# Kernel optimization log

Hardware: AMD Instinct MI355X
Metric: run time of the kernel (lower is better)

Reference implementation:

```python
import jax, jax.numpy as jnp
import numpy as np

N = 100000      # nodes
E = 1200000     # edges per relation
R = 3           # relations
D_IN = 64       # input_dim
HEAD = 4
HD = 16         # output_dim per head
HHD = HEAD * HD # head * output_dim
NEG_SLOPE = 0.01  # torch LeakyReLU default


def setup_inputs() -> dict:
    key = jax.random.key(0)
    ks = jax.random.split(key, 12)
    sc = 0.05
    h = jax.random.normal(ks[0], (N, D_IN), dtype=jnp.float32)
    src = jax.random.randint(ks[1], (R, E), 0, N, dtype=jnp.int32)
    dst = jax.random.randint(ks[2], (R, E), 0, N, dtype=jnp.int32)
    # shared RelationAware d_liner
    d_w = jax.random.normal(ks[3], (D_IN, HHD), dtype=jnp.float32) * sc
    d_b = jnp.zeros((HHD,), jnp.float32)
    # per-relation H_layer w_liner
    w_w = jax.random.normal(ks[4], (R, D_IN, HHD), dtype=jnp.float32) * sc
    w_b = jnp.zeros((R, HHD), jnp.float32)
    # per-relation attention Linear(3*hd, 1)
    atten_w = jax.random.normal(ks[5], (R, 3 * HD), dtype=jnp.float32) * sc
    atten_b = jnp.zeros((R,), jnp.float32)
    # per-relation Gate beta: (2*head*hd, 1)
    beta = jax.random.normal(ks[6], (R, 2 * HHD), dtype=jnp.float32) * sc
    # final combine liner: (R*head*hd -> head*hd)
    lin_w = jax.random.normal(ks[7], (R * HHD, HHD), dtype=jnp.float32) * sc
    lin_b = jnp.zeros((HHD,), jnp.float32)
    return dict(h=h, src=src, dst=dst, d_w=d_w, d_b=d_b, w_w=w_w, w_b=w_b,
                atten_w=atten_w, atten_b=atten_b, beta=beta, lin_w=lin_w, lin_b=lin_b)


def _relation(h, d_feat, s, t, w_w_r, w_b_r, atten_w_r, atten_b_r, beta_r):
    # H_layer forward for one relation; s/t are edge src/dst indices [E]
    hp = h @ w_w_r + w_b_r                       # [N, HHD] (w_liner)
    # RelationAware: tanh(src + dst + (src - dst)) == tanh(2*src)
    es = jnp.tanh(2.0 * d_feat[s])               # [E, HHD] per-edge edge_sum
    src_h = hp[s].reshape(E, HEAD, HD)
    dst_h = hp[t].reshape(E, HEAD, HD)
    es_h = es.reshape(E, HEAD, HD)
    # atten Linear(3*hd,1) on concat[src,dst,edge_s]: split weight, avoid concat
    wa = atten_w_r.reshape(3, HD)
    logits = src_h @ wa[0] + dst_h @ wa[1] + es_h @ wa[2] + atten_b_r  # [E, HEAD]
    alpha = jnp.where(logits >= 0, logits, NEG_SLOPE * logits)          # leaky_relu
    # segment softmax over incoming edges per destination, per head
    amax = jnp.full((N, HEAD), jnp.finfo(jnp.float32).min, jnp.float32).at[t].max(alpha)
    ex = jnp.exp(alpha - amax[t])                                        # [E, HEAD]
    denom = jax.ops.segment_sum(ex, t, num_segments=N)                   # [N, HEAD]
    w = ex / jnp.maximum(denom[t], 1e-20)
    out = jax.ops.segment_sum(w[..., None] * src_h, t, num_segments=N)   # [N, HEAD, HD]
    out = out.reshape(N, HHD)
    # mean of edge_sum over incoming edges per destination
    cnt = jax.ops.segment_sum(jnp.ones((E,), jnp.float32), t, num_segments=N)
    es_node = jax.ops.segment_sum(es, t, num_segments=N) / jnp.maximum(cnt, 1.0)[:, None]
    # Gate
    gate = jax.nn.sigmoid(jnp.concatenate([es_node, out], axis=1) @ beta_r[:, None])  # [N,1]
    return gate * out + (1.0 - gate) * hp


def reference(h, src, dst, d_w, d_b, w_w, w_b, atten_w, atten_b, beta, lin_w, lin_b):
    d_feat = h @ d_w + d_b                        # shared RelationAware d_liner, [N, HHD]
    hs = [
        _relation(h, d_feat, src[r], dst[r], w_w[r], w_b[r], atten_w[r], atten_b[r], beta[r])
        for r in range(R)
    ]
    x = jnp.concatenate(hs, axis=1)               # [N, R*HHD]; dropout p=0 -> identity
    return x @ lin_w + lin_b                      # [N, HHD]
```

## Files before the change

### kernel.cpp

```cpp
#include <hip/hip_runtime.h>

#define N_NODES 100000
#define N_EDGES 1200000
#define R_REL 3
#define RN (R_REL * N_NODES)
#define RE (R_REL * N_EDGES)

#define B_BITS 9
#define W_BKT 512
#define NB_R 196
#define K_BKT (R_REL * NB_R)
#define TILE_A 8192
#define NBLK_A ((RE + TILE_A - 1) / TILE_A)
#define NODE_BLKS 1024

typedef _Float16 half4v __attribute__((ext_vector_type(4)));

__device__ __forceinline__ float bcast(float v, int l) {
  return __int_as_float(__builtin_amdgcn_readlane(__float_as_int(v), l));
}

__device__ __forceinline__ int rel_of(int e) {
  return (e >= 2 * N_EDGES) ? 2 : (e >= N_EDGES ? 1 : 0);
}

__global__ __launch_bounds__(256) void k_hist(const int* __restrict__ dst,
                                              int* __restrict__ tot) {
  __shared__ int sh[K_BKT];
  int tid = threadIdx.x;
  for (int i = tid; i < K_BKT; i += 256) sh[i] = 0;
  __syncthreads();
  int base = blockIdx.x * TILE_A;
  int end = min(base + TILE_A, RE);
  for (int e = base + tid; e < end; e += 256) {
    atomicAdd(&sh[rel_of(e) * NB_R + (dst[e] >> B_BITS)], 1);
  }
  __syncthreads();
  for (int i = tid; i < K_BKT; i += 256) {
    int c = sh[i];
    if (c) atomicAdd(&tot[i], c);
  }
}

__global__ void k_scanK(const int* __restrict__ tot, int* __restrict__ BB,
                        int* __restrict__ cursor) {
  __shared__ int sd[256];
  int t = threadIdx.x;
  int v[3];
  int tots = 0;
#pragma unroll
  for (int q = 0; q < 3; q++) {
    int k = t * 3 + q;
    v[q] = (k < K_BKT) ? tot[k] : 0;
    tots += v[q];
  }
  sd[t] = tots;
  __syncthreads();
  for (int off = 1; off < 256; off <<= 1) {
    int x = (t >= off) ? sd[t - off] : 0;
    __syncthreads();
    sd[t] += x;
    __syncthreads();
  }
  int run = sd[t] - tots;
#pragma unroll
  for (int q = 0; q < 3; q++) {
    int k = t * 3 + q;
    if (k < K_BKT) {
      BB[k] = run;
      cursor[k] = run;
    }
    run += v[q];
  }
  if (t == 255) BB[K_BKT] = RE;
}

__global__ __launch_bounds__(256) void k_scatterA(const int* __restrict__ src,
                                                  const int* __restrict__ dst,
                                                  int* __restrict__ cursor,
                                                  unsigned int* __restrict__ rec) {
  __shared__ int sh[K_BKT];
  int tid = threadIdx.x;
  for (int i = tid; i < K_BKT; i += 256) sh[i] = 0;
  __syncthreads();
  int base = blockIdx.x * TILE_A;
  int end = min(base + TILE_A, RE);
  for (int e = base + tid; e < end; e += 256) {
    atomicAdd(&sh[rel_of(e) * NB_R + (dst[e] >> B_BITS)], 1);
  }
  __syncthreads();
  for (int i = tid; i < K_BKT; i += 256) {
    int c = sh[i];
    sh[i] = c ? atomicAdd(&cursor[i], c) : 0;
  }
  __syncthreads();
  for (int e = base + tid; e < end; e += 256) {
    int d = dst[e];
    int k = rel_of(e) * NB_R + (d >> B_BITS);
    int p = atomicAdd(&sh[k], 1);
    rec[p] = ((unsigned)src[e] << B_BITS) | (unsigned)(d & (W_BKT - 1));
  }
}

__global__ __launch_bounds__(256) void k_nb(
    const unsigned int* __restrict__ rec, const int* __restrict__ BB,
    int* __restrict__ P, int* __restrict__ ssrc,
    const float* __restrict__ h, const float* __restrict__ d_w,
    const float* __restrict__ d_b, const float* __restrict__ w_w,
    const float* __restrict__ w_b, const float* __restrict__ atten_w,
    const float* __restrict__ atten_b, const float* __restrict__ beta,
    _Float16* __restrict__ hp16, float* __restrict__ pk,
    float* __restrict__ adst) {
  __shared__ float sW[4 * 4096];
  __shared__ int cnt[W_BKT];
  __shared__ int sdx[256];
  int tid = threadIdx.x;
  if (blockIdx.x < K_BKT) {
    int kb = blockIdx.x;
    int r = kb / NB_R;
    int nb0 = (kb % NB_R) * W_BKT;
    int beg = BB[kb], end = BB[kb + 1];
    cnt[tid] = 0;
    cnt[256 + tid] = 0;
    __syncthreads();
    for (int e = beg + tid; e < end; e += 256)
      atomicAdd(&cnt[rec[e] & (W_BKT - 1)], 1);
    __syncthreads();
    int v0 = cnt[2 * tid], v1 = cnt[2 * tid + 1];
    int tot2 = v0 + v1;
    sdx[tid] = tot2;
    __syncthreads();
    for (int off = 1; off < 256; off <<= 1) {
      int x = (tid >= off) ? sdx[tid - off] : 0;
      __syncthreads();
      sdx[tid] += x;
      __syncthreads();
    }
    int run = sdx[tid] - tot2;
    int node0 = nb0 + 2 * tid;
    int pbase = r * N_NODES + node0;
    if (node0 < N_NODES) P[pbase] = beg + run;
    if (node0 + 1 < N_NODES) P[pbase + 1] = beg + run + v0;
    cnt[2 * tid] = beg + run;
    cnt[2 * tid + 1] = beg + run + v0;
    __syncthreads();
    for (int e = beg + tid; e < end; e += 256) {
      unsigned rc = rec[e];
      int p = atomicAdd(&cnt[rc & (W_BKT - 1)], 1);
      ssrc[p] = (int)(rc >> B_BITS);
    }
    return;
  }
  int nbid = blockIdx.x - K_BKT;
  for (int idx = tid; idx < 4096; idx += 256) {
    sW[idx] = d_w[idx];
    sW[4096 + idx] = w_w[idx];
    sW[8192 + idx] = w_w[4096 + idx];
    sW[12288 + idx] = w_w[8192 + idx];
  }
  __syncthreads();
  int lane = tid & 63, wid = tid >> 6;
  int wave = nbid * 4 + wid, nw = NODE_BLKS * 4;
  int k16 = lane & 15, hgrp = lane >> 4;
  float dbv = d_b[lane];
  float wbv0 = w_b[lane], wbv1 = w_b[64 + lane], wbv2 = w_b[128 + lane];
  float wa0[3], wa1[3], wa2[3], ab[3], bb[3];
#pragma unroll
  for (int r = 0; r < 3; r++) {
    wa0[r] = atten_w[r * 48 + k16];
    wa1[r] = atten_w[r * 48 + 16 + k16];
    wa2[r] = atten_w[r * 48 + 32 + k16];
    ab[r] = atten_b[r];
    bb[r] = beta[r * 128 + lane];
  }
  for (int g = wave; g < N_NODES / 8; g += nw) {
    int n0 = g * 8;
    float hr[8];
#pragma unroll
    for (int i = 0; i < 8; i++) hr[i] = h[(n0 + i) * 64 + lane];
    float acc[8][4];
#pragma unroll
    for (int i = 0; i < 8; i++) {
      acc[i][0] = dbv; acc[i][1] = wbv0; acc[i][2] = wbv1; acc[i][3] = wbv2;
    }
#pragma unroll 4
    for (int k = 0; k < 64; k++) {
      float w0 = sW[k * 64 + lane];
      float w1 = sW[4096 + k * 64 + lane];
      float w2 = sW[8192 + k * 64 + lane];
      float w3 = sW[12288 + k * 64 + lane];
#pragma unroll
      for (int i = 0; i < 8; i++) {
        float a = bcast(hr[i], k);
        acc[i][0] += a * w0; acc[i][1] += a * w1;
        acc[i][2] += a * w2; acc[i][3] += a * w3;
      }
    }
#pragma unroll
    for (int i = 0; i < 8; i++) {
      int n = n0 + i;
      float esv = tanhf(2.f * acc[i][0]);
#pragma unroll
      for (int r = 0; r < 3; r++) {
        int idxrn = r * N_NODES + n;
        float hpv = acc[i][1 + r];
        hp16[(size_t)idxrn * 64 + lane] = (_Float16)hpv;
        float cs = hpv * wa0[r] + esv * wa2[r];
        float cd = hpv * wa1[r];
#pragma unroll
        for (int m = 1; m < 16; m <<= 1) {
          cs += __shfl_xor(cs, m);
          cd += __shfl_xor(cd, m);
        }
        float sv = esv * bb[r];
#pragma unroll
        for (int m = 1; m < 64; m <<= 1) sv += __shfl_xor(sv, m);
        if (k16 == 0) {
          float2 rec2 = make_float2(cs + ab[r], sv);
          *reinterpret_cast<float2*>(&pk[(size_t)idxrn * 8 + hgrp * 2]) = rec2;
          adst[(size_t)idxrn * 4 + hgrp] = cd;
        }
      }
    }
  }
}

#define EDGE_BODY(EE, OA, DS, SD)                                          \
  {                                                                        \
    int s_ = ssrc[EE];                                                     \
    float2 pv_ = *reinterpret_cast<const float2*>(&pkr[s_ * 8 + head2]);   \
    half4v hv_ = *reinterpret_cast<const half4v*>(&hpr16[s_ * 64 + cq]);   \
    float a_ = pv_.x + adh;                                                \
    a_ = a_ >= 0.f ? a_ : 0.01f * a_;                                      \
    float ex_ = __expf(a_);                                                \
    OA.x += ex_ * (float)hv_.x;                                            \
    OA.y += ex_ * (float)hv_.y;                                            \
    OA.z += ex_ * (float)hv_.z;                                            \
    OA.w += ex_ * (float)hv_.w;                                            \
    DS += ex_;                                                             \
    SD += pv_.y;                                                           \
  }

__global__ __launch_bounds__(1024, 2) void k_fused(
    const _Float16* __restrict__ hp16, const float* __restrict__ pk,
    const float* __restrict__ adst, const int* __restrict__ P,
    const int* __restrict__ ssrc, const float* __restrict__ beta,
    const float* __restrict__ lin_w, const float* __restrict__ lin_b,
    float* __restrict__ out) {
  __shared__ __align__(16) float sLW[64 * 196];
  __shared__ __align__(16) float sHR[16][4][64];
  int tid = threadIdx.x;
  for (int idx = tid; idx < 192 * 64; idx += 1024) {
    int j = idx >> 6, c = idx & 63;
    sLW[c * 196 + j] = lin_w[idx];
  }
  __syncthreads();
  int lane = tid & 63, wid = tid >> 6;
  int g = blockIdx.x * 16 + wid;
  int slot = lane >> 4;
  int c16 = lane & 15;
  int cq = c16 * 4;
  int head = c16 >> 2;
  int head2 = head * 2;
  float y0 = lin_b[lane];
  float y[4] = {y0, y0, y0, y0};
  for (int r = 0; r < 3; r++) {
    const _Float16* __restrict__ hpr16 = hp16 + (size_t)r * N_NODES * 64;
    const float* __restrict__ pkr = pk + (size_t)r * N_NODES * 8;
    float4 b1v = *reinterpret_cast<const float4*>(&beta[r * 128 + 64 + cq]);
#pragma unroll
    for (int i = 0; i < 4; i++) {
      int n = g * 4 + i;
      n = n < N_NODES ? n : N_NODES - 1;
      int idxrn = r * N_NODES + n;
      int beg = P[idxrn];
      int end = (idxrn + 1 < RN) ? P[idxrn + 1] : RE;
      float adh = adst[idxrn * 4 + head];
      half4v hq_ = *reinterpret_cast<const half4v*>(&hpr16[n * 64 + cq]);
      float4 hpv = make_float4((float)hq_.x, (float)hq_.y, (float)hq_.z,
                               (float)hq_.w);
      float4 oaA = {0.f, 0.f, 0.f, 0.f}, oaB = {0.f, 0.f, 0.f, 0.f};
      float dsA = 0.f, dsB = 0.f, sdA = 0.f, sdB = 0.f;
      int e = beg + slot;
      for (; e + 4 < end; e += 8) {
        EDGE_BODY(e, oaA, dsA, sdA);
        EDGE_BODY(e + 4, oaB, dsB, sdB);
      }
      if (e < end) EDGE_BODY(e, oaA, dsA, sdA);
      float4 oa;
      oa.x = oaA.x + oaB.x;
      oa.y = oaA.y + oaB.y;
      oa.z = oaA.z + oaB.z;
      oa.w = oaA.w + oaB.w;
      float ds = dsA + dsB, sd = sdA + sdB;
      oa.x += __shfl_xor(oa.x, 16); oa.x += __shfl_xor(oa.x, 32);
      oa.y += __shfl_xor(oa.y, 16); oa.y += __shfl_xor(oa.y, 32);
      oa.z += __shfl_xor(oa.z, 16); oa.z += __shfl_xor(oa.z, 32);
      oa.w += __shfl_xor(oa.w, 16); oa.w += __shfl_xor(oa.w, 32);
      ds += __shfl_xor(ds, 16); ds += __shfl_xor(ds, 32);
      sd += __shfl_xor(sd, 16); sd += __shfl_xor(sd, 32);
      float inv = 1.f / fmaxf(ds, 1e-20f);
      float4 ov;
      ov.x = oa.x * inv; ov.y = oa.y * inv; ov.z = oa.z * inv; ov.w = oa.w * inv;
      float em = sd / fmaxf((float)(end - beg), 1.f);
      float gc = ov.x * b1v.x + ov.y * b1v.y + ov.z * b1v.z + ov.w * b1v.w;
      gc += __shfl_xor(gc, 1); gc += __shfl_xor(gc, 2);
      gc += __shfl_xor(gc, 4); gc += __shfl_xor(gc, 8);
      float gt = 1.f / (1.f + __expf(-(gc + em)));
      float4 hrv;
      hrv.x = gt * ov.x + (1.f - gt) * hpv.x;
      hrv.y = gt * ov.y + (1.f - gt) * hpv.y;
      hrv.z = gt * ov.z + (1.f - gt) * hpv.z;
      hrv.w = gt * ov.w + (1.f - gt) * hpv.w;
      if (slot == 0) *reinterpret_cast<float4*>(&sHR[wid][i][cq]) = hrv;
    }
    __builtin_amdgcn_wave_barrier();
    const float* wrow = &sLW[lane * 196 + r * 64];
    const float* hrow = &sHR[wid][0][0];
#pragma unroll
    for (int j4 = 0; j4 < 64; j4 += 4) {
      float4 wv = *reinterpret_cast<const float4*>(wrow + j4);
#pragma unroll
      for (int i = 0; i < 4; i++) {
        float4 hv = *reinterpret_cast<const float4*>(hrow + i * 64 + j4);
        y[i] += hv.x * wv.x + hv.y * wv.y + hv.z * wv.z + hv.w * wv.w;
      }
    }
    __builtin_amdgcn_wave_barrier();
  }
#pragma unroll
  for (int i = 0; i < 4; i++) {
    int n = g * 4 + i;
    if (n < N_NODES) out[n * 64 + lane] = y[i];
  }
}

extern "C" void kernel_launch(void* const* d_in, const int* in_sizes, int n_in,
                              void* d_out, int out_size, void* d_ws, size_t ws_size,
                              hipStream_t stream) {
  const float* h = (const float*)d_in[0];
  const int* src = (const int*)d_in[1];
  const int* dst = (const int*)d_in[2];
  const float* d_w = (const float*)d_in[3];
  const float* d_b = (const float*)d_in[4];
  const float* w_w = (const float*)d_in[5];
  const float* w_b = (const float*)d_in[6];
  const float* atten_w = (const float*)d_in[7];
  const float* atten_b = (const float*)d_in[8];
  const float* beta = (const float*)d_in[9];
  const float* lin_w = (const float*)d_in[10];
  const float* lin_b = (const float*)d_in[11];
  float* out = (float*)d_out;

  _Float16* hp16 = (_Float16*)d_ws;
  float* pk = (float*)(hp16 + (size_t)RN * 64);
  float* adst = pk + (size_t)RN * 8;
  int* P = (int*)(adst + (size_t)RN * 4);
  int* ssrc = P + RN;
  unsigned int* rec = (unsigned int*)(ssrc + RE);
  int* tot = (int*)(rec + RE);
  int* BB = tot + K_BKT;
  int* cursor = BB + K_BKT + 1;

  hipMemsetAsync(tot, 0, K_BKT * sizeof(int), stream);
  k_hist<<<NBLK_A, 256, 0, stream>>>(dst, tot);
  k_scanK<<<1, 256, 0, stream>>>(tot, BB, cursor);
  k_scatterA<<<NBLK_A, 256, 0, stream>>>(src, dst, cursor, rec);
  k_nb<<<K_BKT + NODE_BLKS, 256, 0, stream>>>(rec, BB, P, ssrc, h, d_w, d_b,
                                              w_w, w_b, atten_w, atten_b, beta,
                                              hp16, pk, adst);
  int nfb = (N_NODES + 63) / 64;
  k_fused<<<nfb, 1024, 0, stream>>>(hp16, pk, adst, P, ssrc, beta, lin_w,
                                    lin_b, out);
}
```

Measured before the change: 580.9 us.

## Fuse bucket scatter with node projection and sort per-node edges in shared memory

The second-level per-node sort (k_nb bucket blocks writing P and ssrc) is removed. Each k_fused block instead scans its 512-node bucket's records, keeps the ones for its 64 nodes, and builds a local CSR in shared memory. The global scatter now runs as extra blocks inside the node-projection kernel, which cuts one launch and avoids writing and reading back P and ssrc. In exchange, every fused block reads the whole bucket, about 8x redundant record reads, and the shared edge list is capped at 1536 entries, which could overflow on skewed degree distributions.

```diff
diff --git a/kernel.cpp b/kernel.cpp
--- a/kernel.cpp
+++ b/kernel.cpp
@@ -13,6 +13,7 @@
 #define TILE_A 8192
 #define NBLK_A ((RE + TILE_A - 1) / TILE_A)
 #define NODE_BLKS 1024
+#define EL_CAP 1536
 
 typedef _Float16 half4v __attribute__((ext_vector_type(4)));
 
@@ -75,36 +76,9 @@
   if (t == 255) BB[K_BKT] = RE;
 }
 
-__global__ __launch_bounds__(256) void k_scatterA(const int* __restrict__ src,
-                                                  const int* __restrict__ dst,
-                                                  int* __restrict__ cursor,
-                                                  unsigned int* __restrict__ rec) {
-  __shared__ int sh[K_BKT];
-  int tid = threadIdx.x;
-  for (int i = tid; i < K_BKT; i += 256) sh[i] = 0;
-  __syncthreads();
-  int base = blockIdx.x * TILE_A;
-  int end = min(base + TILE_A, RE);
-  for (int e = base + tid; e < end; e += 256) {
-    atomicAdd(&sh[rel_of(e) * NB_R + (dst[e] >> B_BITS)], 1);
-  }
-  __syncthreads();
-  for (int i = tid; i < K_BKT; i += 256) {
-    int c = sh[i];
-    sh[i] = c ? atomicAdd(&cursor[i], c) : 0;
-  }
-  __syncthreads();
-  for (int e = base + tid; e < end; e += 256) {
-    int d = dst[e];
-    int k = rel_of(e) * NB_R + (d >> B_BITS);
-    int p = atomicAdd(&sh[k], 1);
-    rec[p] = ((unsigned)src[e] << B_BITS) | (unsigned)(d & (W_BKT - 1));
-  }
-}
-
-__global__ __launch_bounds__(256) void k_nb(
-    const unsigned int* __restrict__ rec, const int* __restrict__ BB,
-    int* __restrict__ P, int* __restrict__ ssrc,
+__global__ __launch_bounds__(256) void k_sn(
+    const int* __restrict__ src, const int* __restrict__ dst,
+    int* __restrict__ cursor, unsigned int* __restrict__ rec,
     const float* __restrict__ h, const float* __restrict__ d_w,
     const float* __restrict__ d_b, const float* __restrict__ w_w,
     const float* __restrict__ w_b, const float* __restrict__ atten_w,
@@ -112,46 +86,31 @@
     _Float16* __restrict__ hp16, float* __restrict__ pk,
     float* __restrict__ adst) {
   __shared__ float sW[4 * 4096];
-  __shared__ int cnt[W_BKT];
-  __shared__ int sdx[256];
+  __shared__ int sh[K_BKT];
   int tid = threadIdx.x;
-  if (blockIdx.x < K_BKT) {
-    int kb = blockIdx.x;
-    int r = kb / NB_R;
-    int nb0 = (kb % NB_R) * W_BKT;
-    int beg = BB[kb], end = BB[kb + 1];
-    cnt[tid] = 0;
-    cnt[256 + tid] = 0;
-    __syncthreads();
-    for (int e = beg + tid; e < end; e += 256)
-      atomicAdd(&cnt[rec[e] & (W_BKT - 1)], 1);
-    __syncthreads();
-    int v0 = cnt[2 * tid], v1 = cnt[2 * tid + 1];
-    int tot2 = v0 + v1;
-    sdx[tid] = tot2;
-    __syncthreads();
-    for (int off = 1; off < 256; off <<= 1) {
-      int x = (tid >= off) ? sdx[tid - off] : 0;
-      __syncthreads();
-      sdx[tid] += x;
-      __syncthreads();
-    }
-    int run = sdx[tid] - tot2;
-    int node0 = nb0 + 2 * tid;
-    int pbase = r * N_NODES + node0;
-    if (node0 < N_NODES) P[pbase] = beg + run;
-    if (node0 + 1 < N_NODES) P[pbase + 1] = beg + run + v0;
-    cnt[2 * tid] = beg + run;
-    cnt[2 * tid + 1] = beg + run + v0;
-    __syncthreads();
-    for (int e = beg + tid; e < end; e += 256) {
-      unsigned rc = rec[e];
-      int p = atomicAdd(&cnt[rc & (W_BKT - 1)], 1);
-      ssrc[p] = (int)(rc >> B_BITS);
+  if (blockIdx.x < NBLK_A) {
+    for (int i = tid; i < K_BKT; i += 256) sh[i] = 0;
+    __syncthreads();
+    int base = blockIdx.x * TILE_A;
+    int end = min(base + TILE_A, RE);
+    for (int e = base + tid; e < end; e += 256) {
+      atomicAdd(&sh[rel_of(e) * NB_R + (dst[e] >> B_BITS)], 1);
+    }
+    __syncthreads();
+    for (int i = tid; i < K_BKT; i += 256) {
+      int c = sh[i];
+      sh[i] = c ? atomicAdd(&cursor[i], c) : 0;
+    }
+    __syncthreads();
+    for (int e = base + tid; e < end; e += 256) {
+      int d = dst[e];
+      int k = rel_of(e) * NB_R + (d >> B_BITS);
+      int p = atomicAdd(&sh[k], 1);
+      rec[p] = ((unsigned)src[e] << B_BITS) | (unsigned)(d & (W_BKT - 1));
     }
     return;
   }
-  int nbid = blockIdx.x - K_BKT;
+  int nbid = blockIdx.x - NBLK_A;
   for (int idx = tid; idx < 4096; idx += 256) {
     sW[idx] = d_w[idx];
     sW[4096 + idx] = w_w[idx];
@@ -227,7 +186,7 @@
 
 #define EDGE_BODY(EE, OA, DS, SD)                                          \
   {                                                                        \
-    int s_ = ssrc[EE];                                                     \
+    int s_ = eL[EE];                                                       \
     float2 pv_ = *reinterpret_cast<const float2*>(&pkr[s_ * 8 + head2]);   \
     half4v hv_ = *reinterpret_cast<const half4v*>(&hpr16[s_ * 64 + cq]);   \
     float a_ = pv_.x + adh;                                                \
@@ -243,20 +202,23 @@
 
 __global__ __launch_bounds__(1024, 2) void k_fused(
     const _Float16* __restrict__ hp16, const float* __restrict__ pk,
-    const float* __restrict__ adst, const int* __restrict__ P,
-    const int* __restrict__ ssrc, const float* __restrict__ beta,
+    const float* __restrict__ adst, const unsigned int* __restrict__ rec,
+    const int* __restrict__ BB, const float* __restrict__ beta,
     const float* __restrict__ lin_w, const float* __restrict__ lin_b,
     float* __restrict__ out) {
   __shared__ __align__(16) float sLW[64 * 196];
   __shared__ __align__(16) float sHR[16][4][64];
+  __shared__ int eL[EL_CAP];
+  __shared__ int offs[65];
+  __shared__ int cur[64];
   int tid = threadIdx.x;
   for (int idx = tid; idx < 192 * 64; idx += 1024) {
     int j = idx >> 6, c = idx & 63;
     sLW[c * 196 + j] = lin_w[idx];
   }
-  __syncthreads();
   int lane = tid & 63, wid = tid >> 6;
-  int g = blockIdx.x * 16 + wid;
+  int base = blockIdx.x * 64;
+  int bloc = base & (W_BKT - 1);
   int slot = lane >> 4;
   int c16 = lane & 15;
   int cq = c16 * 4;
@@ -268,25 +230,58 @@
     const _Float16* __restrict__ hpr16 = hp16 + (size_t)r * N_NODES * 64;
     const float* __restrict__ pkr = pk + (size_t)r * N_NODES * 8;
     float4 b1v = *reinterpret_cast<const float4*>(&beta[r * 128 + 64 + cq]);
+    int kb = r * NB_R + (base >> B_BITS);
+    int beg = BB[kb], end = BB[kb + 1];
+    __syncthreads();
+    if (tid < 64) cur[tid] = 0;
+    __syncthreads();
+    for (int e = beg + tid; e < end; e += 1024) {
+      unsigned rc = rec[e];
+      int nl = (int)(rc & (W_BKT - 1)) - bloc;
+      if ((unsigned)nl < 64u) atomicAdd(&cur[nl], 1);
+    }
+    __syncthreads();
+    if (wid == 0) {
+      int v = cur[lane];
+      int s = v;
+#pragma unroll
+      for (int off = 1; off < 64; off <<= 1) {
+        int x = __shfl_up(s, off);
+        if (lane >= off) s += x;
+      }
+      offs[lane + 1] = s;
+      if (lane == 0) offs[0] = 0;
+      cur[lane] = s - v;
+    }
+    __syncthreads();
+    for (int e = beg + tid; e < end; e += 1024) {
+      unsigned rc = rec[e];
+      int nl = (int)(rc & (W_BKT - 1)) - bloc;
+      if ((unsigned)nl < 64u) {
+        int p = atomicAdd(&cur[nl], 1);
+        eL[p] = (int)(rc >> B_BITS);
+      }
+    }
+    __syncthreads();
 #pragma unroll
     for (int i = 0; i < 4; i++) {
-      int n = g * 4 + i;
+      int n = base + wid * 4 + i;
       n = n < N_NODES ? n : N_NODES - 1;
+      int nl = n - base;
+      int beg_l = offs[nl], end_l = offs[nl + 1];
       int idxrn = r * N_NODES + n;
-      int beg = P[idxrn];
-      int end = (idxrn + 1 < RN) ? P[idxrn + 1] : RE;
       float adh = adst[idxrn * 4 + head];
       half4v hq_ = *reinterpret_cast<const half4v*>(&hpr16[n * 64 + cq]);
       float4 hpv = make_float4((float)hq_.x, (float)hq_.y, (float)hq_.z,
                                (float)hq_.w);
       float4 oaA = {0.f, 0.f, 0.f, 0.f}, oaB = {0.f, 0.f, 0.f, 0.f};
       float dsA = 0.f, dsB = 0.f, sdA = 0.f, sdB = 0.f;
-      int e = beg + slot;
-      for (; e + 4 < end; e += 8) {
+      int e = beg_l + slot;
+      for (; e + 4 < end_l; e += 8) {
         EDGE_BODY(e, oaA, dsA, sdA);
         EDGE_BODY(e + 4, oaB, dsB, sdB);
       }
-      if (e < end) EDGE_BODY(e, oaA, dsA, sdA);
+      if (e < end_l) EDGE_BODY(e, oaA, dsA, sdA);
       float4 oa;
       oa.x = oaA.x + oaB.x;
       oa.y = oaA.y + oaB.y;
@@ -302,7 +297,7 @@
       float inv = 1.f / fmaxf(ds, 1e-20f);
       float4 ov;
       ov.x = oa.x * inv; ov.y = oa.y * inv; ov.z = oa.z * inv; ov.w = oa.w * inv;
-      float em = sd / fmaxf((float)(end - beg), 1.f);
+      float em = sd / fmaxf((float)(end_l - beg_l), 1.f);
       float gc = ov.x * b1v.x + ov.y * b1v.y + ov.z * b1v.z + ov.w * b1v.w;
       gc += __shfl_xor(gc, 1); gc += __shfl_xor(gc, 2);
       gc += __shfl_xor(gc, 4); gc += __shfl_xor(gc, 8);
@@ -330,7 +325,7 @@
   }
 #pragma unroll
   for (int i = 0; i < 4; i++) {
-    int n = g * 4 + i;
+    int n = base + wid * 4 + i;
     if (n < N_NODES) out[n * 64 + lane] = y[i];
   }
 }
@@ -355,9 +350,7 @@
   _Float16* hp16 = (_Float16*)d_ws;
   float* pk = (float*)(hp16 + (size_t)RN * 64);
   float* adst = pk + (size_t)RN * 8;
-  int* P = (int*)(adst + (size_t)RN * 4);
-  int* ssrc = P + RN;
-  unsigned int* rec = (unsigned int*)(ssrc + RE);
+  unsigned int* rec = (unsigned int*)(adst + (size_t)RN * 4);
   int* tot = (int*)(rec + RE);
   int* BB = tot + K_BKT;
   int* cursor = BB + K_BKT + 1;
@@ -365,11 +358,10 @@
   hipMemsetAsync(tot, 0, K_BKT * sizeof(int), stream);
   k_hist<<<NBLK_A, 256, 0, stream>>>(dst, tot);
   k_scanK<<<1, 256, 0, stream>>>(tot, BB, cursor);
-  k_scatterA<<<NBLK_A, 256, 0, stream>>>(src, dst, cursor, rec);
-  k_nb<<<K_BKT + NODE_BLKS, 256, 0, stream>>>(rec, BB, P, ssrc, h, d_w, d_b,
-                                              w_w, w_b, atten_w, atten_b, beta,
-                                              hp16, pk, adst);
+  k_sn<<<NBLK_A + NODE_BLKS, 256, 0, stream>>>(src, dst, cursor, rec, h, d_w,
+                                               d_b, w_w, w_b, atten_w, atten_b,
+                                               beta, hp16, pk, adst);
   int nfb = (N_NODES + 63) / 64;
-  k_fused<<<nfb, 1024, 0, stream>>>(hp16, pk, adst, P, ssrc, beta, lin_w,
+  k_fused<<<nfb, 1024, 0, stream>>>(hp16, pk, adst, rec, BB, beta, lin_w,
                                     lin_b, out);
 }
```

Result: slower. 642.0 us (+10.5%).
